# Kernel optimization log

Measured on AMD Instinct MI355X. Metric: run time of the kernel, lower is better.

The kernel has to match this reference:

```python
import jax, jax.numpy as jnp
import numpy as np

N_NODES = 100000
N_EDGES = 640000
IN_FEATS = 128
OUT_FEATS = 128


def setup_inputs() -> dict:
    key = jax.random.key(0)
    k1, k2, k3, k4 = jax.random.split(key, 4)
    feature = jax.random.normal(k1, (N_NODES, IN_FEATS), dtype=jnp.float32)
    edge_index = jax.random.randint(k2, (2, N_EDGES), 0, N_NODES, dtype=jnp.int64)
    # Linear params (W stored as [in, out] so out = h @ W + b, same math as torch Linear)
    W = jax.random.normal(k3, (IN_FEATS, OUT_FEATS), dtype=jnp.float32) / np.sqrt(IN_FEATS)
    b = jax.random.normal(k4, (OUT_FEATS,), dtype=jnp.float32) * 0.01
    return {"feature": feature, "edge_index": edge_index, "W": W, "b": b}


def reference(feature, edge_index, W, b):
    src, dst = edge_index[0], edge_index[1]
    # copy_src: gather source-node features along edges -> [E, in]
    msgs = feature[src]
    # sum reduce at destination nodes -> [N, in]
    h = jax.ops.segment_sum(msgs, dst, num_segments=N_NODES)
    # post-aggregation linear
    return h @ W + b
```

## Files before the change

kernel.cpp:

```cpp
#include <hip/hip_runtime.h>

#define N_NODES 100000
#define N_EDGES 640000
#define FEATS   128

typedef __attribute__((ext_vector_type(8))) short short8;
typedef __attribute__((ext_vector_type(4))) float f32x4;

static __device__ __forceinline__ unsigned short f2bf(float f) {
  union { float f; unsigned u; } c; c.f = f;
  unsigned u = c.u + 0x7fffu + ((c.u >> 16) & 1u);
  return (unsigned short)(u >> 16);
}
static __device__ __forceinline__ float asf(unsigned u) {
  union { unsigned u; float f; } c; c.u = u;
  return c.f;
}

__global__ __launch_bounds__(256) void prep_kernel(
    const float* __restrict__ feature, const float* __restrict__ W,
    unsigned short* __restrict__ feat_bf, unsigned short* __restrict__ WT,
    int* __restrict__ cnt) {
  int b = blockIdx.x;
  if (b < 6250) {
    size_t g = (size_t)b * 256 + threadIdx.x;
    const float4* s = (const float4*)feature + g * 2;
    float4 a = s[0], c = s[1];
    unsigned short o[8] = {f2bf(a.x), f2bf(a.y), f2bf(a.z), f2bf(a.w),
                           f2bf(c.x), f2bf(c.y), f2bf(c.z), f2bf(c.w)};
    *(short8*)(feat_bf + g * 8) = *(const short8*)o;
  } else if (b < 6314) {
    int g = (b - 6250) * 256 + threadIdx.x;
    int k = g >> 7, n = g & 127;
    WT[n * 128 + k] = f2bf(W[g]);
  } else {
    int idx = (b - 6314) * 256 + threadIdx.x;
    if (idx < N_NODES / 4) ((int4*)cnt)[idx] = make_int4(0, 0, 0, 0);
  }
}


__global__ __launch_bounds__(256) void hist_kernel(
    const int* __restrict__ edge, int* __restrict__ cnt) {
  int e = blockIdx.x * 256 + threadIdx.x;
  if (e < N_EDGES) atomicAdd(&cnt[edge[N_EDGES + e]], 1);
}

__global__ __launch_bounds__(256) void scan_block(
    const int* __restrict__ cnt, int* __restrict__ off,
    int* __restrict__ bsum, int n) {
  __shared__ int tmp[256];
  int gid = blockIdx.x * 256 + threadIdx.x;
  int v = (gid < n) ? cnt[gid] : 0;
  tmp[threadIdx.x] = v;
  __syncthreads();
  #pragma unroll
  for (int ofs = 1; ofs < 256; ofs <<= 1) {
    int t = (threadIdx.x >= ofs) ? tmp[threadIdx.x - ofs] : 0;
    __syncthreads();
    tmp[threadIdx.x] += t;
    __syncthreads();
  }
  if (gid < n) off[gid] = tmp[threadIdx.x] - v;
  if (threadIdx.x == 255) bsum[blockIdx.x] = tmp[255];
}

__global__ __launch_bounds__(256) void add_offsets(
    int* __restrict__ off, int* __restrict__ cur,
    const int* __restrict__ bsum, int n) {
  __shared__ int wsum[4];
  int s = 0;
  for (int j = threadIdx.x; j < blockIdx.x; j += 256) s += bsum[j];
  #pragma unroll
  for (int o = 32; o > 0; o >>= 1) s += __shfl_down(s, o);
  if ((threadIdx.x & 63) == 0) wsum[threadIdx.x >> 6] = s;
  __syncthreads();
  int base = wsum[0] + wsum[1] + wsum[2] + wsum[3];
  int gid = blockIdx.x * 256 + threadIdx.x;
  if (gid < n) {
    int o = off[gid] + base;
    off[gid] = o;
    cur[gid] = o;
  }
}

__global__ __launch_bounds__(256) void fill_csr(
    const int* __restrict__ edge, int* __restrict__ cur,
    int* __restrict__ csr) {
  int e = blockIdx.x * 256 + threadIdx.x;
  if (e < N_EDGES) {
    int d = edge[N_EDGES + e];
    int p = atomicAdd(&cur[d], 1);
    csr[p] = edge[e];
  }
}

__global__ __launch_bounds__(256) void aggregate_kernel(
    const unsigned short* __restrict__ feat,
    const int* __restrict__ off, const int* __restrict__ cnt,
    const int* __restrict__ csr, unsigned short* __restrict__ h) {
  int g    = blockIdx.x * 256 + threadIdx.x;
  int node = g >> 4;
  int lane = g & 15;
  if (node >= N_NODES) return;
  int start = off[node];
  int deg   = cnt[node];

  float a0 = 0.f, a1 = 0.f, a2 = 0.f, a3 = 0.f;
  float a4 = 0.f, a5 = 0.f, a6 = 0.f, a7 = 0.f;

  int i = 0;
  for (; i + 1 < deg; i += 2) {
    int s0 = csr[start + i];
    int s1 = csr[start + i + 1];
    uint4 p = *(const uint4*)(feat + (size_t)s0 * FEATS + lane * 8);
    uint4 q = *(const uint4*)(feat + (size_t)s1 * FEATS + lane * 8);
    a0 += asf(p.x << 16) + asf(q.x << 16);
    a1 += asf(p.x & 0xffff0000u) + asf(q.x & 0xffff0000u);
    a2 += asf(p.y << 16) + asf(q.y << 16);
    a3 += asf(p.y & 0xffff0000u) + asf(q.y & 0xffff0000u);
    a4 += asf(p.z << 16) + asf(q.z << 16);
    a5 += asf(p.z & 0xffff0000u) + asf(q.z & 0xffff0000u);
    a6 += asf(p.w << 16) + asf(q.w << 16);
    a7 += asf(p.w & 0xffff0000u) + asf(q.w & 0xffff0000u);
  }
  if (i < deg) {
    int s = csr[start + i];
    uint4 p = *(const uint4*)(feat + (size_t)s * FEATS + lane * 8);
    a0 += asf(p.x << 16);
    a1 += asf(p.x & 0xffff0000u);
    a2 += asf(p.y << 16);
    a3 += asf(p.y & 0xffff0000u);
    a4 += asf(p.z << 16);
    a5 += asf(p.z & 0xffff0000u);
    a6 += asf(p.w << 16);
    a7 += asf(p.w & 0xffff0000u);
  }

  uint4 o;
  o.x = (unsigned)f2bf(a0) | ((unsigned)f2bf(a1) << 16);
  o.y = (unsigned)f2bf(a2) | ((unsigned)f2bf(a3) << 16);
  o.z = (unsigned)f2bf(a4) | ((unsigned)f2bf(a5) << 16);
  o.w = (unsigned)f2bf(a6) | ((unsigned)f2bf(a7) << 16);
  *(uint4*)(h + (size_t)node * FEATS + lane * 8) = o;
}


#define LDSK 136

__global__ __launch_bounds__(256) void gemm_mfma(
    const unsigned short* __restrict__ hbf,
    const unsigned short* __restrict__ WT,
    const float* __restrict__ bias,
    float* __restrict__ out) {
  __shared__ unsigned short WTs[128 * LDSK];

  #pragma unroll
  for (int i = 0; i < 8; ++i) {
    int c = threadIdx.x + i * 256;
    int n = c >> 4, j = c & 15;
    *(short8*)&WTs[n * LDSK + j * 8] = *(const short8*)(WT + n * 128 + j * 8);
  }
  __syncthreads();

  const int w    = threadIdx.x >> 6;
  const int lane = threadIdx.x & 63;
  const int ln15 = lane & 15;
  const int quad = lane >> 4;
  const int row_base = blockIdx.x * 128 + w * 32;

  f32x4 acc[2][8] = {};

  #pragma unroll
  for (int kb = 0; kb < 4; ++kb) {
    int kofs = kb * 32 + quad * 8;
    short8 a0 = *(const short8*)(hbf + (size_t)(row_base + ln15) * FEATS + kofs);
    short8 a1 = *(const short8*)(hbf + (size_t)(row_base + 16 + ln15) * FEATS + kofs);
    #pragma unroll
    for (int ct = 0; ct < 8; ++ct) {
      short8 b = *(const short8*)&WTs[(ct * 16 + ln15) * LDSK + kofs];
      acc[0][ct] = __builtin_amdgcn_mfma_f32_16x16x32_bf16(a0, b, acc[0][ct], 0, 0, 0);
      acc[1][ct] = __builtin_amdgcn_mfma_f32_16x16x32_bf16(a1, b, acc[1][ct], 0, 0, 0);
    }
  }

  #pragma unroll
  for (int t = 0; t < 2; ++t) {
    #pragma unroll
    for (int ct = 0; ct < 8; ++ct) {
      int col = ct * 16 + ln15;
      float bv = bias[col];
      #pragma unroll
      for (int r = 0; r < 4; ++r) {
        int row = row_base + t * 16 + quad * 4 + r;
        if (row < N_NODES)
          out[(size_t)row * FEATS + col] = acc[t][ct][r] + bv;
      }
    }
  }
}


extern "C" void kernel_launch(void* const* d_in, const int* in_sizes, int n_in,
                              void* d_out, int out_size, void* d_ws, size_t ws_size,
                              hipStream_t stream) {
  const float* feature = (const float*)d_in[0];
  const int*   edge    = (const int*)d_in[1];
  const float* W       = (const float*)d_in[2];
  const float* bias    = (const float*)d_in[3];
  float*       out     = (float*)d_out;

  char* ws = (char*)d_ws;
  int* cnt  = (int*)(ws);
  int* off  = (int*)(ws + (512  << 10));
  int* cur  = (int*)(ws + (1024 << 10));
  int* bsum = (int*)(ws + (1536 << 10));
  int* csr  = (int*)(ws + (1600 << 10));
  unsigned short* WT      = (unsigned short*)(ws + (4300  << 10));
  unsigned short* feat_bf = (unsigned short*)(ws + (4400  << 10));
  unsigned short* h_bf    = (unsigned short*)(ws + (30000 << 10));

  const int NB = (N_NODES + 255) / 256;

  prep_kernel<<<6412, 256, 0, stream>>>(feature, W, feat_bf, WT, cnt);

  hist_kernel<<<(N_EDGES + 255) / 256, 256, 0, stream>>>(edge, cnt);
  scan_block<<<NB, 256, 0, stream>>>(cnt, off, bsum, N_NODES);
  add_offsets<<<NB, 256, 0, stream>>>(off, cur, bsum, N_NODES);
  fill_csr<<<(N_EDGES + 255) / 256, 256, 0, stream>>>(edge, cur, csr);

  aggregate_kernel<<<(N_NODES * 16 + 255) / 256, 256, 0, stream>>>(
      feat_bf, off, cnt, csr, h_bf);

  gemm_mfma<<<(N_NODES + 127) / 128, 256, 0, stream>>>(h_bf, WT, bias, out);
}
```

Before: 209.4 us.

## Fuse CSR build into persistent kernel and aggregation with GEMM

The five preprocessing kernels (bf16 conversion, histogram, two scan phases, CSR fill) become one persistent 512-block kernel separated by software grid barriers. Aggregation and the MFMA GEMM are merged so the aggregated rows stay in LDS in bf16 instead of going through a global buffer. This removes several launches and the global write and read of h. In exchange, the grid barriers depend on all 512 blocks being resident at once and on a self-resetting barrier counter. The fused agg+GEMM kernel also uses more LDS per block, which can lower occupancy for the latency-bound gather.

```diff
diff --git a/kernel.cpp b/kernel.cpp
--- a/kernel.cpp
+++ b/kernel.cpp
@@ -3,6 +3,8 @@
 #define N_NODES 100000
 #define N_EDGES 640000
 #define FEATS   128
+#define GRID1   512
+#define NB      391
 
 typedef __attribute__((ext_vector_type(8))) short short8;
 typedef __attribute__((ext_vector_type(4))) float f32x4;
@@ -17,168 +19,172 @@
   return c.f;
 }
 
-__global__ __launch_bounds__(256) void prep_kernel(
+__device__ __forceinline__ void grid_barrier(int* bar) {
+  __syncthreads();
+  if (threadIdx.x == 0) {
+    __threadfence();
+    atomicCAS(bar, (int)0xAAAAAAAAu, 0);
+    atomicAdd(bar, 1);
+    while (__hip_atomic_load(bar, __ATOMIC_RELAXED, __HIP_MEMORY_SCOPE_AGENT) < GRID1)
+      __builtin_amdgcn_s_sleep(8);
+  }
+  __syncthreads();
+  __threadfence();
+}
+
+__global__ __launch_bounds__(256, 4) void build_kernel(
     const float* __restrict__ feature, const float* __restrict__ W,
+    const int* __restrict__ edge,
     unsigned short* __restrict__ feat_bf, unsigned short* __restrict__ WT,
-    int* __restrict__ cnt) {
-  int b = blockIdx.x;
-  if (b < 6250) {
-    size_t g = (size_t)b * 256 + threadIdx.x;
-    const float4* s = (const float4*)feature + g * 2;
+    int* __restrict__ cnt, int* __restrict__ off, int* __restrict__ cur,
+    int* __restrict__ bsum, int* __restrict__ csr, int* __restrict__ bars) {
+  __shared__ int tmp[256];
+  __shared__ int wsum[4];
+  const int tid  = threadIdx.x;
+  const int gtid = blockIdx.x * 256 + tid;
+  const int gstr = GRID1 * 256;
+
+  for (int i = gtid; i < N_NODES * FEATS / 8; i += gstr) {
+    const float4* s = (const float4*)feature + (size_t)i * 2;
     float4 a = s[0], c = s[1];
     unsigned short o[8] = {f2bf(a.x), f2bf(a.y), f2bf(a.z), f2bf(a.w),
                            f2bf(c.x), f2bf(c.y), f2bf(c.z), f2bf(c.w)};
-    *(short8*)(feat_bf + g * 8) = *(const short8*)o;
-  } else if (b < 6314) {
-    int g = (b - 6250) * 256 + threadIdx.x;
-    int k = g >> 7, n = g & 127;
-    WT[n * 128 + k] = f2bf(W[g]);
-  } else {
-    int idx = (b - 6314) * 256 + threadIdx.x;
-    if (idx < N_NODES / 4) ((int4*)cnt)[idx] = make_int4(0, 0, 0, 0);
-  }
-}
-
-
-__global__ __launch_bounds__(256) void hist_kernel(
-    const int* __restrict__ edge, int* __restrict__ cnt) {
-  int e = blockIdx.x * 256 + threadIdx.x;
-  if (e < N_EDGES) atomicAdd(&cnt[edge[N_EDGES + e]], 1);
-}
-
-__global__ __launch_bounds__(256) void scan_block(
-    const int* __restrict__ cnt, int* __restrict__ off,
-    int* __restrict__ bsum, int n) {
-  __shared__ int tmp[256];
-  int gid = blockIdx.x * 256 + threadIdx.x;
-  int v = (gid < n) ? cnt[gid] : 0;
-  tmp[threadIdx.x] = v;
-  __syncthreads();
-  #pragma unroll
-  for (int ofs = 1; ofs < 256; ofs <<= 1) {
-    int t = (threadIdx.x >= ofs) ? tmp[threadIdx.x - ofs] : 0;
+    *(short8*)(feat_bf + (size_t)i * 8) = *(const short8*)o;
+  }
+  for (int i = gtid; i < FEATS * FEATS; i += gstr) {
+    int k = i >> 7, n = i & 127;
+    WT[n * 128 + k] = f2bf(W[i]);
+  }
+  for (int i = gtid; i < N_NODES / 4; i += gstr)
+    ((int4*)cnt)[i] = make_int4(0, 0, 0, 0);
+  grid_barrier(bars + 0);
+
+  for (int e = gtid; e < N_EDGES; e += gstr)
+    atomicAdd(&cnt[edge[N_EDGES + e]], 1);
+  grid_barrier(bars + 1);
+
+  if (blockIdx.x < NB) {
+    int gid = blockIdx.x * 256 + tid;
+    int v = (gid < N_NODES) ? cnt[gid] : 0;
+    tmp[tid] = v;
     __syncthreads();
-    tmp[threadIdx.x] += t;
+    #pragma unroll
+    for (int ofs = 1; ofs < 256; ofs <<= 1) {
+      int t = (tid >= ofs) ? tmp[tid - ofs] : 0;
+      __syncthreads();
+      tmp[tid] += t;
+      __syncthreads();
+    }
+    if (gid < N_NODES) off[gid] = tmp[tid] - v;
+    if (tid == 255) bsum[blockIdx.x] = tmp[255];
+  }
+  grid_barrier(bars + 2);
+
+  if (blockIdx.x < NB) {
+    int s = 0;
+    for (int j = tid; j < blockIdx.x; j += 256) s += bsum[j];
+    #pragma unroll
+    for (int o = 32; o > 0; o >>= 1) s += __shfl_down(s, o);
+    if ((tid & 63) == 0) wsum[tid >> 6] = s;
     __syncthreads();
-  }
-  if (gid < n) off[gid] = tmp[threadIdx.x] - v;
-  if (threadIdx.x == 255) bsum[blockIdx.x] = tmp[255];
-}
-
-__global__ __launch_bounds__(256) void add_offsets(
-    int* __restrict__ off, int* __restrict__ cur,
-    const int* __restrict__ bsum, int n) {
-  __shared__ int wsum[4];
-  int s = 0;
-  for (int j = threadIdx.x; j < blockIdx.x; j += 256) s += bsum[j];
-  #pragma unroll
-  for (int o = 32; o > 0; o >>= 1) s += __shfl_down(s, o);
-  if ((threadIdx.x & 63) == 0) wsum[threadIdx.x >> 6] = s;
-  __syncthreads();
-  int base = wsum[0] + wsum[1] + wsum[2] + wsum[3];
-  int gid = blockIdx.x * 256 + threadIdx.x;
-  if (gid < n) {
-    int o = off[gid] + base;
-    off[gid] = o;
-    cur[gid] = o;
-  }
-}
-
-__global__ __launch_bounds__(256) void fill_csr(
-    const int* __restrict__ edge, int* __restrict__ cur,
-    int* __restrict__ csr) {
-  int e = blockIdx.x * 256 + threadIdx.x;
-  if (e < N_EDGES) {
+    int base = wsum[0] + wsum[1] + wsum[2] + wsum[3];
+    int gid = blockIdx.x * 256 + tid;
+    if (gid < N_NODES) {
+      int o = off[gid] + base;
+      off[gid] = o;
+      cur[gid] = o;
+    }
+  }
+  grid_barrier(bars + 3);
+
+  for (int e = gtid; e < N_EDGES; e += gstr) {
     int d = edge[N_EDGES + e];
     int p = atomicAdd(&cur[d], 1);
     csr[p] = edge[e];
   }
 }
 
-__global__ __launch_bounds__(256) void aggregate_kernel(
+__global__ __launch_bounds__(256, 2) void agg_gemm(
     const unsigned short* __restrict__ feat,
     const int* __restrict__ off, const int* __restrict__ cnt,
-    const int* __restrict__ csr, unsigned short* __restrict__ h) {
-  int g    = blockIdx.x * 256 + threadIdx.x;
-  int node = g >> 4;
-  int lane = g & 15;
-  if (node >= N_NODES) return;
-  int start = off[node];
-  int deg   = cnt[node];
-
-  float a0 = 0.f, a1 = 0.f, a2 = 0.f, a3 = 0.f;
-  float a4 = 0.f, a5 = 0.f, a6 = 0.f, a7 = 0.f;
-
-  int i = 0;
-  for (; i + 1 < deg; i += 2) {
-    int s0 = csr[start + i];
-    int s1 = csr[start + i + 1];
-    uint4 p = *(const uint4*)(feat + (size_t)s0 * FEATS + lane * 8);
-    uint4 q = *(const uint4*)(feat + (size_t)s1 * FEATS + lane * 8);
-    a0 += asf(p.x << 16) + asf(q.x << 16);
-    a1 += asf(p.x & 0xffff0000u) + asf(q.x & 0xffff0000u);
-    a2 += asf(p.y << 16) + asf(q.y << 16);
-    a3 += asf(p.y & 0xffff0000u) + asf(q.y & 0xffff0000u);
-    a4 += asf(p.z << 16) + asf(q.z << 16);
-    a5 += asf(p.z & 0xffff0000u) + asf(q.z & 0xffff0000u);
-    a6 += asf(p.w << 16) + asf(q.w << 16);
-    a7 += asf(p.w & 0xffff0000u) + asf(q.w & 0xffff0000u);
-  }
-  if (i < deg) {
-    int s = csr[start + i];
-    uint4 p = *(const uint4*)(feat + (size_t)s * FEATS + lane * 8);
-    a0 += asf(p.x << 16);
-    a1 += asf(p.x & 0xffff0000u);
-    a2 += asf(p.y << 16);
-    a3 += asf(p.y & 0xffff0000u);
-    a4 += asf(p.z << 16);
-    a5 += asf(p.z & 0xffff0000u);
-    a6 += asf(p.w << 16);
-    a7 += asf(p.w & 0xffff0000u);
-  }
-
-  uint4 o;
-  o.x = (unsigned)f2bf(a0) | ((unsigned)f2bf(a1) << 16);
-  o.y = (unsigned)f2bf(a2) | ((unsigned)f2bf(a3) << 16);
-  o.z = (unsigned)f2bf(a4) | ((unsigned)f2bf(a5) << 16);
-  o.w = (unsigned)f2bf(a6) | ((unsigned)f2bf(a7) << 16);
-  *(uint4*)(h + (size_t)node * FEATS + lane * 8) = o;
-}
-
-
-#define LDSK 136
-
-__global__ __launch_bounds__(256) void gemm_mfma(
-    const unsigned short* __restrict__ hbf,
+    const int* __restrict__ csr,
     const unsigned short* __restrict__ WT,
     const float* __restrict__ bias,
     float* __restrict__ out) {
-  __shared__ unsigned short WTs[128 * LDSK];
+  __shared__ unsigned short hs[16 * 128 * 8];
+  __shared__ unsigned short wf[16 * 128 * 8];
+  const int tid = threadIdx.x;
 
   #pragma unroll
   for (int i = 0; i < 8; ++i) {
-    int c = threadIdx.x + i * 256;
-    int n = c >> 4, j = c & 15;
-    *(short8*)&WTs[n * LDSK + j * 8] = *(const short8*)(WT + n * 128 + j * 8);
+    int c = tid + i * 256;
+    int n = c & 127, kc = c >> 7;
+    *(uint4*)&wf[c * 8] = *(const uint4*)(WT + n * 128 + kc * 8);
+  }
+
+  const int lane16 = tid & 15;
+  const int nl0    = tid >> 4;
+  const int row0   = blockIdx.x * 128;
+
+  for (int r8 = 0; r8 < 8; ++r8) {
+    int node_local = nl0 + r8 * 16;
+    int node = row0 + node_local;
+    float a0 = 0.f, a1 = 0.f, a2 = 0.f, a3 = 0.f;
+    float a4 = 0.f, a5 = 0.f, a6 = 0.f, a7 = 0.f;
+    if (node < N_NODES) {
+      int start = off[node];
+      int deg   = cnt[node];
+      int i = 0;
+      for (; i + 1 < deg; i += 2) {
+        int s0 = csr[start + i];
+        int s1 = csr[start + i + 1];
+        uint4 p = *(const uint4*)(feat + (size_t)s0 * FEATS + lane16 * 8);
+        uint4 q = *(const uint4*)(feat + (size_t)s1 * FEATS + lane16 * 8);
+        a0 += asf(p.x << 16) + asf(q.x << 16);
+        a1 += asf(p.x & 0xffff0000u) + asf(q.x & 0xffff0000u);
+        a2 += asf(p.y << 16) + asf(q.y << 16);
+        a3 += asf(p.y & 0xffff0000u) + asf(q.y & 0xffff0000u);
+        a4 += asf(p.z << 16) + asf(q.z << 16);
+        a5 += asf(p.z & 0xffff0000u) + asf(q.z & 0xffff0000u);
+        a6 += asf(p.w << 16) + asf(q.w << 16);
+        a7 += asf(p.w & 0xffff0000u) + asf(q.w & 0xffff0000u);
+      }
+      if (i < deg) {
+        int s = csr[start + i];
+        uint4 p = *(const uint4*)(feat + (size_t)s * FEATS + lane16 * 8);
+        a0 += asf(p.x << 16);
+        a1 += asf(p.x & 0xffff0000u);
+        a2 += asf(p.y << 16);
+        a3 += asf(p.y & 0xffff0000u);
+        a4 += asf(p.z << 16);
+        a5 += asf(p.z & 0xffff0000u);
+        a6 += asf(p.w << 16);
+        a7 += asf(p.w & 0xffff0000u);
+      }
+    }
+    uint4 o;
+    o.x = (unsigned)f2bf(a0) | ((unsigned)f2bf(a1) << 16);
+    o.y = (unsigned)f2bf(a2) | ((unsigned)f2bf(a3) << 16);
+    o.z = (unsigned)f2bf(a4) | ((unsigned)f2bf(a5) << 16);
+    o.w = (unsigned)f2bf(a6) | ((unsigned)f2bf(a7) << 16);
+    *(uint4*)&hs[(lane16 * 128 + node_local) * 8] = o;
   }
   __syncthreads();
 
-  const int w    = threadIdx.x >> 6;
-  const int lane = threadIdx.x & 63;
+  const int w    = tid >> 6;
+  const int lane = tid & 63;
   const int ln15 = lane & 15;
   const int quad = lane >> 4;
-  const int row_base = blockIdx.x * 128 + w * 32;
 
   f32x4 acc[2][8] = {};
-
   #pragma unroll
   for (int kb = 0; kb < 4; ++kb) {
-    int kofs = kb * 32 + quad * 8;
-    short8 a0 = *(const short8*)(hbf + (size_t)(row_base + ln15) * FEATS + kofs);
-    short8 a1 = *(const short8*)(hbf + (size_t)(row_base + 16 + ln15) * FEATS + kofs);
+    int kc = kb * 4 + quad;
+    short8 a0 = *(const short8*)&hs[(kc * 128 + w * 32 + ln15) * 8];
+    short8 a1 = *(const short8*)&hs[(kc * 128 + w * 32 + 16 + ln15) * 8];
     #pragma unroll
     for (int ct = 0; ct < 8; ++ct) {
-      short8 b = *(const short8*)&WTs[(ct * 16 + ln15) * LDSK + kofs];
+      short8 b = *(const short8*)&wf[(kc * 128 + ct * 16 + ln15) * 8];
       acc[0][ct] = __builtin_amdgcn_mfma_f32_16x16x32_bf16(a0, b, acc[0][ct], 0, 0, 0);
       acc[1][ct] = __builtin_amdgcn_mfma_f32_16x16x32_bf16(a1, b, acc[1][ct], 0, 0, 0);
     }
@@ -192,7 +198,7 @@
       float bv = bias[col];
       #pragma unroll
       for (int r = 0; r < 4; ++r) {
-        int row = row_base + t * 16 + quad * 4 + r;
+        int row = row0 + w * 32 + t * 16 + quad * 4 + r;
         if (row < N_NODES)
           out[(size_t)row * FEATS + col] = acc[t][ct][r] + bv;
       }
@@ -215,22 +221,14 @@
   int* off  = (int*)(ws + (512  << 10));
   int* cur  = (int*)(ws + (1024 << 10));
   int* bsum = (int*)(ws + (1536 << 10));
+  int* bars = (int*)(ws + (1544 << 10));
   int* csr  = (int*)(ws + (1600 << 10));
-  unsigned short* WT      = (unsigned short*)(ws + (4300  << 10));
-  unsigned short* feat_bf = (unsigned short*)(ws + (4400  << 10));
-  unsigned short* h_bf    = (unsigned short*)(ws + (30000 << 10));
-
-  const int NB = (N_NODES + 255) / 256;
-
-  prep_kernel<<<6412, 256, 0, stream>>>(feature, W, feat_bf, WT, cnt);
-
-  hist_kernel<<<(N_EDGES + 255) / 256, 256, 0, stream>>>(edge, cnt);
-  scan_block<<<NB, 256, 0, stream>>>(cnt, off, bsum, N_NODES);
-  add_offsets<<<NB, 256, 0, stream>>>(off, cur, bsum, N_NODES);
-  fill_csr<<<(N_EDGES + 255) / 256, 256, 0, stream>>>(edge, cur, csr);
-
-  aggregate_kernel<<<(N_NODES * 16 + 255) / 256, 256, 0, stream>>>(
-      feat_bf, off, cnt, csr, h_bf);
-
-  gemm_mfma<<<(N_NODES + 127) / 128, 256, 0, stream>>>(h_bf, WT, bias, out);
-}
+  unsigned short* WT      = (unsigned short*)(ws + (4300 << 10));
+  unsigned short* feat_bf = (unsigned short*)(ws + (4400 << 10));
+
+  build_kernel<<<GRID1, 256, 0, stream>>>(
+      feature, W, edge, feat_bf, WT, cnt, off, cur, bsum, csr, bars);
+
+  agg_gemm<<<(N_NODES + 127) / 128, 256, 0, stream>>>(
+      feat_bf, off, cnt, csr, WT, bias, out);
+}
```

Result: slower. 560.0 us (+167.4%).
